# Performance work log

Hardware: AMD Instinct MI355X
Metric: run time of the kernel (lower is better)

## Reference

```python
import jax, jax.numpy as jnp
import numpy as np

EPS = 1e-6

def rmsnorm(x, w):
    # matches torch RMSNorm: normalize in fp32, cast back, scale
    xf = x.astype(jnp.float32)
    n = xf * jax.lax.rsqrt(jnp.mean(xf * xf, axis=-1, keepdims=True) + EPS)
    return n.astype(x.dtype) * w

def swiglu(x, w1, w2, w3):
    # torch Linear convention: weight shape [out, in], y = x @ W.T
    return (jax.nn.silu(x @ w1.T) * (x @ w3.T)) @ w2.T

B, D, E, K = 32768, 1024, 8, 2
NF = 4  # int(8 * 0.5) fractal experts, rest are plain SwiGLU(dim, 4*dim)

def setup_inputs() -> dict:
    key = jax.random.key(0)
    ks = jax.random.split(key, 8)
    def w(k, shape, fan_in):
        return jax.random.normal(k, shape, jnp.float32) * (fan_in ** -0.5)
    return {
        "x": jax.random.normal(ks[0], (B, D), jnp.float32),
        "gate_w": w(ks[1], (E, D), D),
        # FractalBlock experts (depth=1): RMSNorm weight, SwiGLU(dim, 2*dim), LayerScale gamma
        "fr_norm": jnp.ones((NF, D), jnp.float32),
        "fr_gamma": jnp.full((NF, D), 1e-5, jnp.float32),
        "fr_w1": w(ks[2], (NF, 2 * D, D), D),
        "fr_w2": w(ks[3], (NF, D, 2 * D), 2 * D),
        "fr_w3": w(ks[4], (NF, 2 * D, D), D),
        # Plain SwiGLU experts: SwiGLU(dim, 4*dim)
        "sw_w1": w(ks[5], (E - NF, 4 * D, D), D),
        "sw_w2": w(ks[6], (E - NF, D, 4 * D), 4 * D),
        "sw_w3": w(ks[7], (E - NF, 4 * D, D), D),
    }

def reference(x, gate_w, fr_norm, fr_gamma, fr_w1, fr_w2, fr_w3, sw_w1, sw_w2, sw_w3):
    n_experts = gate_w.shape[0]
    n_fractal = fr_w1.shape[0]
    # gating: softmax -> top-k -> renormalize selected weights
    probs = jax.nn.softmax(x @ gate_w.T, axis=-1)            # [B, E]
    tk_w, tk_i = jax.lax.top_k(probs, K)                     # [B, K]
    tk_w = tk_w / jnp.sum(tk_w, axis=-1, keepdims=True)
    # combine weights: zero for unselected experts (math identical to sparse dispatch)
    comb = jnp.sum(jax.nn.one_hot(tk_i, n_experts, dtype=x.dtype) * tk_w[..., None], axis=1)  # [B, E]
    out = jnp.zeros_like(x)
    for e in range(n_experts):  # fixed small structural loop over experts
        if e < n_fractal:
            # FractalBlock(depth=1), eval mode: stochastic depth is identity
            xn = rmsnorm(x, fr_norm[e])
            xn = xn + swiglu(xn, fr_w1[e], fr_w2[e], fr_w3[e])
            eo = fr_gamma[e] * xn + x
        else:
            j = e - n_fractal
            eo = swiglu(x, sw_w1[j], sw_w2[j], sw_w3[j])
        out = out + comb[:, e:e + 1] * eo
    return out
```

## Files before the change

### kernel.cpp

```cpp
#include <hip/hip_runtime.h>
#include <stdint.h>

#define B_TOK 32768
#define DIM   1024
#define NEXP  8
#define NFR   4
#define HF    2048
#define HS    4096
#define CT    64
#define NCH   9
#define PADROWS 66560

typedef __bf16 bf16;
typedef bf16  bf16x8 __attribute__((ext_vector_type(8)));
typedef bf16  bf16x4 __attribute__((ext_vector_type(4)));
typedef float f32x4  __attribute__((ext_vector_type(4)));

#define LDSOFF(R, CC) (((R) << 6) + ((((CC) ^ ((R) & 7))) << 3))

__global__ __launch_bounds__(256) void gate_kernel(
    const float* __restrict__ x, const float* __restrict__ gw_g,
    bf16* __restrict__ xb, float* __restrict__ rms,
    int* __restrict__ top2, float* __restrict__ c12) {
  __shared__ float gw[NEXP * DIM];
  for (int i = threadIdx.x; i < NEXP * DIM / 4; i += 256)
    *(f32x4*)(gw + i * 4) = *(const f32x4*)(gw_g + i * 4);
  __syncthreads();
  const int lane = threadIdx.x & 63;
  const int wave = threadIdx.x >> 6;
  const int row  = blockIdx.x * 4 + wave;
  const float* xr = x + (size_t)row * DIM;
  f32x4 xv[4];
#pragma unroll
  for (int i = 0; i < 4; i++) xv[i] = *(const f32x4*)(xr + lane * 4 + i * 256);
  float ss = 0.f;
  double dot[8] = {0, 0, 0, 0, 0, 0, 0, 0};
#pragma unroll
  for (int i = 0; i < 4; i++) {
#pragma unroll
    for (int c = 0; c < 4; c++) ss += xv[i][c] * xv[i][c];
#pragma unroll
    for (int e = 0; e < 8; e++) {
      const f32x4 g = *(const f32x4*)(gw + e * DIM + i * 256 + lane * 4);
#pragma unroll
      for (int c = 0; c < 4; c++) dot[e] += (double)xv[i][c] * (double)g[c];
    }
  }
#pragma unroll
  for (int off = 32; off > 0; off >>= 1) {
    ss += __shfl_xor(ss, off, 64);
#pragma unroll
    for (int e = 0; e < 8; e++) dot[e] += __shfl_xor(dot[e], off, 64);
  }
  const float rv = 1.0f / sqrtf(ss * (1.0f / DIM) + 1e-6f);
  if (lane == 0) rms[row] = rv;
  int i1 = 0; double m1 = dot[0];
#pragma unroll
  for (int e = 1; e < 8; e++) if (dot[e] > m1) { m1 = dot[e]; i1 = e; }
  int i2 = 0; double m2 = -1e300;
#pragma unroll
  for (int e = 0; e < 8; e++) if (e != i1 && dot[e] > m2) { m2 = dot[e]; i2 = e; }
  const double t  = exp(m2 - m1);
  if (lane == 0) {
    top2[row] = i1 | (i2 << 8);
    c12[2 * row]     = (float)(1.0 / (1.0 + t));
    c12[2 * row + 1] = (float)(t / (1.0 + t));
  }
#pragma unroll
  for (int i = 0; i < 4; i++) {
    bf16x4 o;
#pragma unroll
    for (int c = 0; c < 4; c++) o[c] = (bf16)xv[i][c];
    *(bf16x4*)(xb + (size_t)row * DIM + lane * 4 + i * 256) = o;
  }
}

__global__ __launch_bounds__(1024) void histoff_kernel(
    const int* __restrict__ top2, int* __restrict__ tileOff,
    int* __restrict__ rowOff) {
  __shared__ int h[8];
  if (threadIdx.x < 8) h[threadIdx.x] = 0;
  __syncthreads();
  int c[8] = {0, 0, 0, 0, 0, 0, 0, 0};
  for (int i = 0; i < B_TOK / 1024; i++) {
    const int pk = top2[threadIdx.x + i * 1024];
    const int e1 = pk & 255, e2 = pk >> 8;
#pragma unroll
    for (int e = 0; e < 8; e++) c[e] += (e1 == e) + (e2 == e);
  }
#pragma unroll
  for (int e = 0; e < 8; e++) {
#pragma unroll
    for (int off = 32; off > 0; off >>= 1) c[e] += __shfl_xor(c[e], off, 64);
  }
  if ((threadIdx.x & 63) == 0) {
#pragma unroll
    for (int e = 0; e < 8; e++) atomicAdd(&h[e], c[e]);
  }
  __syncthreads();
  if (threadIdx.x == 0) {
    int t = 0;
    for (int e = 0; e < 8; e++) {
      tileOff[e] = t;
      rowOff[e]  = t * 128;
      t += (h[e] + 127) >> 7;
    }
    tileOff[8] = t;
  }
}

__global__ __launch_bounds__(256) void assign_kernel(
    const int* __restrict__ top2, const float* __restrict__ c12,
    const int* __restrict__ rowOff, int* __restrict__ cur,
    int* __restrict__ perm, float* __restrict__ cwg) {
  __shared__ int lhist[8];
  __shared__ int lbase[8];
  if (threadIdx.x < 8) lhist[threadIdx.x] = 0;
  __syncthreads();
  const int t = blockIdx.x * 256 + threadIdx.x;
  const int pk = top2[t];
  const int e1 = pk & 255, e2 = pk >> 8;
  const int p1 = atomicAdd(&lhist[e1], 1);
  const int p2 = atomicAdd(&lhist[e2], 1);
  __syncthreads();
  if (threadIdx.x < 8) {
    const int c = lhist[threadIdx.x];
    lbase[threadIdx.x] = c ? atomicAdd(&cur[threadIdx.x * 32], c) : 0;
  }
  __syncthreads();
  const int g1 = rowOff[e1] + lbase[e1] + p1;
  perm[g1] = t; cwg[g1] = c12[2 * t];
  const int g2 = rowOff[e2] + lbase[e2] + p2;
  perm[g2] = t; cwg[g2] = c12[2 * t + 1];
}

__global__ __launch_bounds__(256) void cvt_kernel(
    const float* __restrict__ src, bf16* __restrict__ dst, int n4) {
  const int i = blockIdx.x * 256 + threadIdx.x;
  if (i >= n4) return;
  f32x4 v = *(const f32x4*)(src + (size_t)i * 4);
  *(bf16x4*)(dst + (size_t)i * 4) = __builtin_convertvector(v, bf16x4);
}

__global__ __launch_bounds__(256) void cvt_scaled_kernel(
    const float* __restrict__ src, const float* __restrict__ norm,
    bf16* __restrict__ dst, int n4) {
  const int i = blockIdx.x * 256 + threadIdx.x;
  if (i >= n4) return;
  const size_t f = (size_t)i * 4;
  f32x4 v = *(const f32x4*)(src + f);
  const float* np_ = norm + ((f >> 21) << 10) + (f & 1023);
#pragma unroll
  for (int c = 0; c < 4; c++) v[c] *= np_[c];
  *(bf16x4*)(dst + f) = __builtin_convertvector(v, bf16x4);
}

__device__ __forceinline__ void stage_sw(const bf16* __restrict__ g0, int ld,
                                         bf16* s0, int wave, int lane) {
  const int r = lane >> 3;
  const int c = (lane & 7) ^ r;
  const bf16* g = g0 + (size_t)(wave * 32 + r) * ld + c * 8;
  bf16* s = s0 + wave * 2048;
#pragma unroll
  for (int i = 0; i < 4; i++) {
    __builtin_amdgcn_global_load_lds(
        (const __attribute__((address_space(1))) void*)(uintptr_t)(g + (size_t)(i * 8) * ld),
        (__attribute__((address_space(3))) void*)(uintptr_t)(s + i * 512), 16, 0, 0);
  }
}

__global__ __launch_bounds__(256, 2) void gemm1_kernel(
    const bf16* __restrict__ xb, const int* __restrict__ perm,
    const float* __restrict__ rms,
    const bf16* __restrict__ fw1, const bf16* __restrict__ fw3,
    const bf16* __restrict__ s1b, const bf16* __restrict__ s3b,
    const int* __restrict__ tileOff, bf16* __restrict__ G, int chunk) {
  const int bt = chunk * CT + blockIdx.y;
  int toff[9];
#pragma unroll
  for (int i = 0; i < 9; i++) toff[i] = tileOff[i];
  if (bt >= toff[8]) return;
  int e = 0;
#pragma unroll
  for (int i = 1; i < 8; i++) if (bt >= toff[i]) e = i;
  const bool isfr = (e < NFR);
  const int nt = isfr ? 16 : 32;
  if ((int)blockIdx.x >= nt) return;
  const bf16* B1 = isfr ? fw1 + (size_t)e * HF * DIM : s1b + (size_t)(e - NFR) * HS * DIM;
  const bf16* B3 = isfr ? fw3 + (size_t)e * HF * DIM : s3b + (size_t)(e - NFR) * HS * DIM;

  __shared__ __attribute__((aligned(16))) bf16 As[128 * 64];
  __shared__ __attribute__((aligned(16))) bf16 Bs1[128 * 64];
  __shared__ __attribute__((aligned(16))) bf16 Bs3[128 * 64];
  const int lane = threadIdx.x & 63, wave = threadIdx.x >> 6;
  const int wm = wave >> 1, wn = wave & 1;
  const int g0 = bt * 128;
  const int n0 = blockIdx.x * 128;

  const int rA = lane >> 3;
  const int cA = (lane & 7) ^ rA;
  const bf16* Ag[4];
#pragma unroll
  for (int i = 0; i < 4; i++) {
    int tk = perm[g0 + wave * 32 + i * 8 + rA];
    if (tk < 0) tk = 0;
    Ag[i] = xb + (size_t)tk * DIM + cA * 8;
  }
  const bf16* B1b = B1 + (size_t)n0 * DIM;
  const bf16* B3b = B3 + (size_t)n0 * DIM;

  f32x4 acc1[4][4], acc3[4][4];
#pragma unroll
  for (int i = 0; i < 4; i++)
#pragma unroll
    for (int j = 0; j < 4; j++) {
      f32x4 z = {0.f, 0.f, 0.f, 0.f};
      acc1[i][j] = z; acc3[i][j] = z;
    }
  const int lr = lane & 15, lq = lane >> 4;
  bf16* Asw = As + wave * 2048;
  for (int k0 = 0; k0 < DIM; k0 += 64) {
#pragma unroll
    for (int i = 0; i < 4; i++) {
      __builtin_amdgcn_global_load_lds(
          (const __attribute__((address_space(1))) void*)(uintptr_t)(Ag[i] + k0),
          (__attribute__((address_space(3))) void*)(uintptr_t)(Asw + i * 512), 16, 0, 0);
    }
    stage_sw(B1b + k0, DIM, Bs1, wave, lane);
    stage_sw(B3b + k0, DIM, Bs3, wave, lane);
    __syncthreads();
#pragma unroll
    for (int ks = 0; ks < 2; ks++) {
      bf16x8 af[4], bf_[4], cf_[4];
#pragma unroll
      for (int mi = 0; mi < 4; mi++) {
        const int R = wm * 64 + mi * 16 + lr;
        af[mi] = *(const bf16x8*)(As + LDSOFF(R, ks * 4 + lq));
      }
#pragma unroll
      for (int ni = 0; ni < 4; ni++) {
        const int R = wn * 64 + ni * 16 + lr;
        bf_[ni] = *(const bf16x8*)(Bs1 + LDSOFF(R, ks * 4 + lq));
        cf_[ni] = *(const bf16x8*)(Bs3 + LDSOFF(R, ks * 4 + lq));
      }
#pragma unroll
      for (int mi = 0; mi < 4; mi++)
#pragma unroll
        for (int ni = 0; ni < 4; ni++) {
          acc1[mi][ni] = __builtin_amdgcn_mfma_f32_16x16x32_bf16(af[mi], bf_[ni], acc1[mi][ni], 0, 0, 0);
          acc3[mi][ni] = __builtin_amdgcn_mfma_f32_16x16x32_bf16(af[mi], cf_[ni], acc3[mi][ni], 0, 0, 0);
        }
    }
    __syncthreads();
  }
#pragma unroll
  for (int mi = 0; mi < 4; mi++) {
#pragma unroll
    for (int r = 0; r < 4; r++) {
      const int row_l = wm * 64 + mi * 16 + lq * 4 + r;
      float s = 1.0f;
      if (isfr) {
        int tok = perm[g0 + row_l];
        s = rms[tok < 0 ? 0 : tok];
      }
      bf16* Grow = G + (size_t)(blockIdx.y * 128 + row_l) * HS;
#pragma unroll
      for (int ni = 0; ni < 4; ni++) {
        const int col = n0 + wn * 64 + ni * 16 + lr;
        const float h1 = acc1[mi][ni][r] * s;
        const float h3 = acc3[mi][ni][r] * s;
        Grow[col] = (bf16)(h1 / (1.0f + __expf(-h1)) * h3);
      }
    }
  }
}

__global__ __launch_bounds__(256, 2) void gemm2_kernel(
    const bf16* __restrict__ G, const int* __restrict__ perm,
    const float* __restrict__ cwg, const float* __restrict__ rms,
    const float* __restrict__ gamma_all, const float* __restrict__ norm_all,
    const float* __restrict__ x,
    const bf16* __restrict__ fw2, const bf16* __restrict__ s2b,
    const int* __restrict__ tileOff, float* __restrict__ out, int chunk) {
  const int bt = chunk * CT + blockIdx.y;
  int toff[9];
#pragma unroll
  for (int i = 0; i < 9; i++) toff[i] = tileOff[i];
  if (bt >= toff[8]) return;
  int e = 0;
#pragma unroll
  for (int i = 1; i < 8; i++) if (bt >= toff[i]) e = i;
  const bool isfr = (e < NFR);
  const int K = isfr ? HF : HS;
  const bf16* Bw = isfr ? fw2 + (size_t)e * DIM * HF : s2b + (size_t)(e - NFR) * DIM * HS;

  __shared__ __attribute__((aligned(16))) bf16 As[128 * 64];
  __shared__ __attribute__((aligned(16))) bf16 Bs[128 * 64];
  const int lane = threadIdx.x & 63, wave = threadIdx.x >> 6;
  const int wm = wave >> 1, wn = wave & 1;
  const int n0 = blockIdx.x * 128;
  f32x4 acc[4][4];
#pragma unroll
  for (int i = 0; i < 4; i++)
#pragma unroll
    for (int j = 0; j < 4; j++) { f32x4 z = {0.f, 0.f, 0.f, 0.f}; acc[i][j] = z; }
  const bf16* Ab = G + (size_t)(blockIdx.y * 128) * HS;
  const bf16* Bb = Bw + (size_t)n0 * K;
  const int lr = lane & 15, lq = lane >> 4;
  for (int k0 = 0; k0 < K; k0 += 64) {
    stage_sw(Ab + k0, HS, As, wave, lane);
    stage_sw(Bb + k0, K, Bs, wave, lane);
    __syncthreads();
#pragma unroll
    for (int ks = 0; ks < 2; ks++) {
      bf16x8 af[4], bf_[4];
#pragma unroll
      for (int mi = 0; mi < 4; mi++) {
        const int R = wm * 64 + mi * 16 + lr;
        af[mi] = *(const bf16x8*)(As + LDSOFF(R, ks * 4 + lq));
      }
#pragma unroll
      for (int ni = 0; ni < 4; ni++) {
        const int R = wn * 64 + ni * 16 + lr;
        bf_[ni] = *(const bf16x8*)(Bs + LDSOFF(R, ks * 4 + lq));
      }
#pragma unroll
      for (int mi = 0; mi < 4; mi++)
#pragma unroll
        for (int ni = 0; ni < 4; ni++)
          acc[mi][ni] = __builtin_amdgcn_mfma_f32_16x16x32_bf16(af[mi], bf_[ni], acc[mi][ni], 0, 0, 0);
    }
    __syncthreads();
  }
#pragma unroll
  for (int mi = 0; mi < 4; mi++) {
#pragma unroll
    for (int r = 0; r < 4; r++) {
      const int row_l = wm * 64 + mi * 16 + lq * 4 + r;
      const int g_row = bt * 128 + row_l;
      const int tok = perm[g_row];
      if (tok < 0) continue;
      const float cw = cwg[g_row];
      const float rv = rms[tok];
#pragma unroll
      for (int ni = 0; ni < 4; ni++) {
        const int col = n0 + wn * 64 + ni * 16 + lr;
        const float a = acc[mi][ni][r];
        float res;
        if (isfr) {
          const float xvv = x[(size_t)tok * DIM + col];
          res = cw * (gamma_all[e * DIM + col] * (rv * xvv * norm_all[e * DIM + col] + a) + xvv);
        } else {
          res = cw * a;
        }
        atomicAdd(&out[(size_t)tok * DIM + col], res);
      }
    }
  }
}

extern "C" void kernel_launch(void* const* d_in, const int* in_sizes, int n_in,
                              void* d_out, int out_size, void* d_ws, size_t ws_size,
                              hipStream_t stream) {
  const float* x        = (const float*)d_in[0];
  const float* gate_w   = (const float*)d_in[1];
  const float* fr_norm  = (const float*)d_in[2];
  const float* fr_gamma = (const float*)d_in[3];
  const float* fr_w1    = (const float*)d_in[4];
  const float* fr_w2    = (const float*)d_in[5];
  const float* fr_w3    = (const float*)d_in[6];
  const float* sw_w1    = (const float*)d_in[7];
  const float* sw_w2    = (const float*)d_in[8];
  const float* sw_w3    = (const float*)d_in[9];
  float* out = (float*)d_out;

  char* ws = (char*)d_ws;
  bf16*  xb    = (bf16*)(ws);
  bf16*  fw1   = (bf16*)(ws + 67108864);
  bf16*  fw3   = (bf16*)(ws + 83886080);
  bf16*  fw2   = (bf16*)(ws + 100663296);
  bf16*  s1b   = (bf16*)(ws + 117440512);
  bf16*  s3b   = (bf16*)(ws + 150994944);
  bf16*  s2b   = (bf16*)(ws + 184549376);
  bf16*  G     = (bf16*)(ws + 218103808);
  float* rmsb  = (float*)(ws + 285212672);
  int*   top2  = (int*)  (ws + 285343744);
  float* c12   = (float*)(ws + 285474816);
  int*   perm  = (int*)  (ws + 285736960);
  float* cwg   = (float*)(ws + 286003200);
  int*   cur   = (int*)  (ws + 286269440);
  int*   tileOff = (int*)(ws + 286270464);
  int*   rowOff  = (int*)(ws + 286270500);

  hipMemsetAsync(d_out, 0, (size_t)out_size * sizeof(float), stream);
  hipMemsetAsync(cur, 0, 1024, stream);
  hipMemsetAsync(perm, 0xFF, PADROWS * 4, stream);

  gate_kernel<<<B_TOK / 4, 256, 0, stream>>>(x, gate_w, xb, rmsb, top2, c12);
  histoff_kernel<<<1, 1024, 0, stream>>>(top2, tileOff, rowOff);
  assign_kernel<<<B_TOK / 256, 256, 0, stream>>>(top2, c12, rowOff, cur, perm, cwg);

  cvt_scaled_kernel<<<8192, 256, 0, stream>>>(fr_w1, fr_norm, fw1, 2097152);
  cvt_scaled_kernel<<<8192, 256, 0, stream>>>(fr_w3, fr_norm, fw3, 2097152);
  cvt_kernel<<<8192, 256, 0, stream>>>(fr_w2, fw2, 2097152);
  cvt_kernel<<<16384, 256, 0, stream>>>(sw_w1, s1b, 4194304);
  cvt_kernel<<<16384, 256, 0, stream>>>(sw_w3, s3b, 4194304);
  cvt_kernel<<<16384, 256, 0, stream>>>(sw_w2, s2b, 4194304);

  for (int c = 0; c < NCH; c++) {
    gemm1_kernel<<<dim3(32, CT), 256, 0, stream>>>(
        xb, perm, rmsb, fw1, fw3, s1b, s3b, tileOff, G, c);
    gemm2_kernel<<<dim3(8, CT), 256, 0, stream>>>(
        G, perm, cwg, rmsb, fr_gamma, fr_norm, x, fw2, s2b, tileOff, out, c);
  }
}
```

Before: 2.741 ms.

## Interleave W1/W3 weights and use 256x256 double-buffered gemm1 tiles

Weight conversion now interleaves W1 and W3 rows in 16-row blocks into a single matrix, so gemm1 runs one fused GEMM where adjacent column fragments pair up for the SwiGLU epilogue. Gemm1 moves to 512-thread blocks with 256x256 tiles, double-buffered LDS staging and MFMA priority hints, to get more reuse per load and overlap global loads with compute. Expert row padding goes to 256, and gemm2 keeps 128-row tiles through a second offset table. The cost is more LDS and registers per block (32 accumulators per thread), which may lower occupancy, plus extra padding rows.

Result: no change. 2.728 ms (-0.5%).

```diff
diff --git a/kernel.cpp b/kernel.cpp
--- a/kernel.cpp
+++ b/kernel.cpp
@@ -7,9 +7,10 @@
 #define NFR   4
 #define HF    2048
 #define HS    4096
-#define CT    64
+#define CT1   32
+#define CT2   64
 #define NCH   9
-#define PADROWS 66560
+#define PADROWS 67584
 
 typedef __bf16 bf16;
 typedef bf16  bf16x8 __attribute__((ext_vector_type(8)));
@@ -76,8 +77,8 @@
 }
 
 __global__ __launch_bounds__(1024) void histoff_kernel(
-    const int* __restrict__ top2, int* __restrict__ tileOff,
-    int* __restrict__ rowOff) {
+    const int* __restrict__ top2, int* __restrict__ tileOff256,
+    int* __restrict__ tileOff128, int* __restrict__ rowOff) {
   __shared__ int h[8];
   if (threadIdx.x < 8) h[threadIdx.x] = 0;
   __syncthreads();
@@ -101,11 +102,13 @@
   if (threadIdx.x == 0) {
     int t = 0;
     for (int e = 0; e < 8; e++) {
-      tileOff[e] = t;
-      rowOff[e]  = t * 128;
-      t += (h[e] + 127) >> 7;
-    }
-    tileOff[8] = t;
+      tileOff256[e] = t;
+      tileOff128[e] = 2 * t;
+      rowOff[e]     = t * 256;
+      t += (h[e] + 255) >> 8;
+    }
+    tileOff256[8] = t;
+    tileOff128[8] = 2 * t;
   }
 }
 
@@ -142,17 +145,37 @@
   *(bf16x4*)(dst + (size_t)i * 4) = __builtin_convertvector(v, bf16x4);
 }
 
-__global__ __launch_bounds__(256) void cvt_scaled_kernel(
-    const float* __restrict__ src, const float* __restrict__ norm,
-    bf16* __restrict__ dst, int n4) {
+__global__ __launch_bounds__(256) void cvt_inter_fr(
+    const float* __restrict__ w1, const float* __restrict__ w3,
+    const float* __restrict__ norm, bf16* __restrict__ dst) {
   const int i = blockIdx.x * 256 + threadIdx.x;
-  if (i >= n4) return;
-  const size_t f = (size_t)i * 4;
-  f32x4 v = *(const f32x4*)(src + f);
-  const float* np_ = norm + ((f >> 21) << 10) + (f & 1023);
-#pragma unroll
-  for (int c = 0; c < 4; c++) v[c] *= np_[c];
-  *(bf16x4*)(dst + f) = __builtin_convertvector(v, bf16x4);
+  const int col4 = i & 255;
+  const int rp   = (i >> 8) & 4095;
+  const int e    = i >> 20;
+  const int blk  = rp >> 4;
+  const int sr   = ((blk >> 1) << 4) + (rp & 15);
+  const float* src = (blk & 1) ? w3 : w1;
+  f32x4 v  = *(const f32x4*)(src + ((size_t)e * HF + sr) * DIM + col4 * 4);
+  f32x4 nv = *(const f32x4*)(norm + e * DIM + col4 * 4);
+#pragma unroll
+  for (int c = 0; c < 4; c++) v[c] *= nv[c];
+  *(bf16x4*)(dst + ((size_t)e * 4096 + rp) * DIM + col4 * 4) =
+      __builtin_convertvector(v, bf16x4);
+}
+
+__global__ __launch_bounds__(256) void cvt_inter_sw(
+    const float* __restrict__ w1, const float* __restrict__ w3,
+    bf16* __restrict__ dst) {
+  const int i = blockIdx.x * 256 + threadIdx.x;
+  const int col4 = i & 255;
+  const int rp   = (i >> 8) & 8191;
+  const int e    = i >> 21;
+  const int blk  = rp >> 4;
+  const int sr   = ((blk >> 1) << 4) + (rp & 15);
+  const float* src = (blk & 1) ? w3 : w1;
+  f32x4 v = *(const f32x4*)(src + ((size_t)e * HS + sr) * DIM + col4 * 4);
+  *(bf16x4*)(dst + ((size_t)e * 8192 + rp) * DIM + col4 * 4) =
+      __builtin_convertvector(v, bf16x4);
 }
 
 __device__ __forceinline__ void stage_sw(const bf16* __restrict__ g0, int ld,
@@ -169,16 +192,15 @@
   }
 }
 
-__global__ __launch_bounds__(256, 2) void gemm1_kernel(
+__global__ __launch_bounds__(512, 2) void gemm1_kernel(
     const bf16* __restrict__ xb, const int* __restrict__ perm,
     const float* __restrict__ rms,
-    const bf16* __restrict__ fw1, const bf16* __restrict__ fw3,
-    const bf16* __restrict__ s1b, const bf16* __restrict__ s3b,
-    const int* __restrict__ tileOff, bf16* __restrict__ G, int chunk) {
-  const int bt = chunk * CT + blockIdx.y;
+    const bf16* __restrict__ fwi, const bf16* __restrict__ swi,
+    const int* __restrict__ tileOff256, bf16* __restrict__ G, int chunk) {
+  const int bt = chunk * CT1 + blockIdx.y;
   int toff[9];
 #pragma unroll
-  for (int i = 0; i < 9; i++) toff[i] = tileOff[i];
+  for (int i = 0; i < 9; i++) toff[i] = tileOff256[i];
   if (bt >= toff[8]) return;
   int e = 0;
 #pragma unroll
@@ -186,16 +208,15 @@
   const bool isfr = (e < NFR);
   const int nt = isfr ? 16 : 32;
   if ((int)blockIdx.x >= nt) return;
-  const bf16* B1 = isfr ? fw1 + (size_t)e * HF * DIM : s1b + (size_t)(e - NFR) * HS * DIM;
-  const bf16* B3 = isfr ? fw3 + (size_t)e * HF * DIM : s3b + (size_t)(e - NFR) * HS * DIM;
-
-  __shared__ __attribute__((aligned(16))) bf16 As[128 * 64];
-  __shared__ __attribute__((aligned(16))) bf16 Bs1[128 * 64];
-  __shared__ __attribute__((aligned(16))) bf16 Bs3[128 * 64];
+  const bf16* Bp = isfr ? fwi + (size_t)e * 4096 * DIM
+                        : swi + (size_t)(e - NFR) * 8192 * DIM;
+
+  __shared__ __attribute__((aligned(16))) bf16 As[2 * 16384];
+  __shared__ __attribute__((aligned(16))) bf16 Bs[2 * 16384];
   const int lane = threadIdx.x & 63, wave = threadIdx.x >> 6;
-  const int wm = wave >> 1, wn = wave & 1;
-  const int g0 = bt * 128;
-  const int n0 = blockIdx.x * 128;
+  const int wm = wave >> 2, wn = wave & 3;
+  const int g0  = bt * 256;
+  const int n0p = blockIdx.x * 256;
 
   const int rA = lane >> 3;
   const int cA = (lane & 7) ^ rA;
@@ -206,69 +227,81 @@
     if (tk < 0) tk = 0;
     Ag[i] = xb + (size_t)tk * DIM + cA * 8;
   }
-  const bf16* B1b = B1 + (size_t)n0 * DIM;
-  const bf16* B3b = B3 + (size_t)n0 * DIM;
-
-  f32x4 acc1[4][4], acc3[4][4];
-#pragma unroll
-  for (int i = 0; i < 4; i++)
-#pragma unroll
-    for (int j = 0; j < 4; j++) {
-      f32x4 z = {0.f, 0.f, 0.f, 0.f};
-      acc1[i][j] = z; acc3[i][j] = z;
-    }
+  const bf16* Bg = Bp + (size_t)(n0p + wave * 32 + rA) * DIM + cA * 8;
+
+  f32x4 acc[8][4];
+#pragma unroll
+  for (int i = 0; i < 8; i++)
+#pragma unroll
+    for (int j = 0; j < 4; j++) { f32x4 z = {0.f, 0.f, 0.f, 0.f}; acc[i][j] = z; }
   const int lr = lane & 15, lq = lane >> 4;
-  bf16* Asw = As + wave * 2048;
-  for (int k0 = 0; k0 < DIM; k0 += 64) {
+
+  auto stage = [&](int buf, int k0) {
+    bf16* sa = As + buf * 16384 + wave * 2048;
+    bf16* sb = Bs + buf * 16384 + wave * 2048;
 #pragma unroll
     for (int i = 0; i < 4; i++) {
       __builtin_amdgcn_global_load_lds(
           (const __attribute__((address_space(1))) void*)(uintptr_t)(Ag[i] + k0),
-          (__attribute__((address_space(3))) void*)(uintptr_t)(Asw + i * 512), 16, 0, 0);
-    }
-    stage_sw(B1b + k0, DIM, Bs1, wave, lane);
-    stage_sw(B3b + k0, DIM, Bs3, wave, lane);
-    __syncthreads();
+          (__attribute__((address_space(3))) void*)(uintptr_t)(sa + i * 512), 16, 0, 0);
+    }
+#pragma unroll
+    for (int i = 0; i < 4; i++) {
+      __builtin_amdgcn_global_load_lds(
+          (const __attribute__((address_space(1))) void*)(uintptr_t)(Bg + (size_t)(i * 8) * DIM + k0),
+          (__attribute__((address_space(3))) void*)(uintptr_t)(sb + i * 512), 16, 0, 0);
+    }
+  };
+  auto compute = [&](int buf) {
+    const bf16* Ab = As + buf * 16384;
+    const bf16* Bb = Bs + buf * 16384;
 #pragma unroll
     for (int ks = 0; ks < 2; ks++) {
-      bf16x8 af[4], bf_[4], cf_[4];
-#pragma unroll
-      for (int mi = 0; mi < 4; mi++) {
-        const int R = wm * 64 + mi * 16 + lr;
-        af[mi] = *(const bf16x8*)(As + LDSOFF(R, ks * 4 + lq));
-      }
-#pragma unroll
-      for (int ni = 0; ni < 4; ni++) {
-        const int R = wn * 64 + ni * 16 + lr;
-        bf_[ni] = *(const bf16x8*)(Bs1 + LDSOFF(R, ks * 4 + lq));
-        cf_[ni] = *(const bf16x8*)(Bs3 + LDSOFF(R, ks * 4 + lq));
-      }
-#pragma unroll
-      for (int mi = 0; mi < 4; mi++)
-#pragma unroll
-        for (int ni = 0; ni < 4; ni++) {
-          acc1[mi][ni] = __builtin_amdgcn_mfma_f32_16x16x32_bf16(af[mi], bf_[ni], acc1[mi][ni], 0, 0, 0);
-          acc3[mi][ni] = __builtin_amdgcn_mfma_f32_16x16x32_bf16(af[mi], cf_[ni], acc3[mi][ni], 0, 0, 0);
-        }
-    }
-    __syncthreads();
-  }
-#pragma unroll
-  for (int mi = 0; mi < 4; mi++) {
+      bf16x8 af[8], bfv[4];
+#pragma unroll
+      for (int mi = 0; mi < 8; mi++)
+        af[mi] = *(const bf16x8*)(Ab + LDSOFF(wm * 128 + mi * 16 + lr, ks * 4 + lq));
+#pragma unroll
+      for (int ni = 0; ni < 4; ni++)
+        bfv[ni] = *(const bf16x8*)(Bb + LDSOFF(wn * 64 + ni * 16 + lr, ks * 4 + lq));
+      __builtin_amdgcn_s_setprio(1);
+#pragma unroll
+      for (int mi = 0; mi < 8; mi++)
+#pragma unroll
+        for (int ni = 0; ni < 4; ni++)
+          acc[mi][ni] = __builtin_amdgcn_mfma_f32_16x16x32_bf16(af[mi], bfv[ni], acc[mi][ni], 0, 0, 0);
+      __builtin_amdgcn_s_setprio(0);
+    }
+  };
+
+  stage(0, 0);
+  __syncthreads();
+  int k = 64;
+#pragma unroll 1
+  for (int t = 0; t < 7; t++) {
+    stage(1, k); compute(0); __syncthreads(); k += 64;
+    stage(0, k); compute(1); __syncthreads(); k += 64;
+  }
+  stage(1, k); compute(0); __syncthreads();
+  compute(1);
+
+  const int gh = n0p >> 1;
+#pragma unroll
+  for (int mi = 0; mi < 8; mi++) {
 #pragma unroll
     for (int r = 0; r < 4; r++) {
-      const int row_l = wm * 64 + mi * 16 + lq * 4 + r;
+      const int row_l = wm * 128 + mi * 16 + lq * 4 + r;
       float s = 1.0f;
       if (isfr) {
         int tok = perm[g0 + row_l];
         s = rms[tok < 0 ? 0 : tok];
       }
-      bf16* Grow = G + (size_t)(blockIdx.y * 128 + row_l) * HS;
-#pragma unroll
-      for (int ni = 0; ni < 4; ni++) {
-        const int col = n0 + wn * 64 + ni * 16 + lr;
-        const float h1 = acc1[mi][ni][r] * s;
-        const float h3 = acc3[mi][ni][r] * s;
+      bf16* Grow = G + (size_t)(blockIdx.y * 256 + row_l) * HS;
+#pragma unroll
+      for (int nh = 0; nh < 2; nh++) {
+        const float h1 = acc[mi][2 * nh][r] * s;
+        const float h3 = acc[mi][2 * nh + 1][r] * s;
+        const int col = gh + wn * 32 + nh * 16 + lr;
         Grow[col] = (bf16)(h1 / (1.0f + __expf(-h1)) * h3);
       }
     }
@@ -281,11 +314,11 @@
     const float* __restrict__ gamma_all, const float* __restrict__ norm_all,
     const float* __restrict__ x,
     const bf16* __restrict__ fw2, const bf16* __restrict__ s2b,
-    const int* __restrict__ tileOff, float* __restrict__ out, int chunk) {
-  const int bt = chunk * CT + blockIdx.y;
+    const int* __restrict__ tileOff128, float* __restrict__ out, int chunk) {
+  const int bt = chunk * CT2 + blockIdx.y;
   int toff[9];
 #pragma unroll
-  for (int i = 0; i < 9; i++) toff[i] = tileOff[i];
+  for (int i = 0; i < 9; i++) toff[i] = tileOff128[i];
   if (bt >= toff[8]) return;
   int e = 0;
 #pragma unroll
@@ -376,41 +409,38 @@
 
   char* ws = (char*)d_ws;
   bf16*  xb    = (bf16*)(ws);
-  bf16*  fw1   = (bf16*)(ws + 67108864);
-  bf16*  fw3   = (bf16*)(ws + 83886080);
+  bf16*  fwi   = (bf16*)(ws + 67108864);
   bf16*  fw2   = (bf16*)(ws + 100663296);
-  bf16*  s1b   = (bf16*)(ws + 117440512);
-  bf16*  s3b   = (bf16*)(ws + 150994944);
+  bf16*  swi   = (bf16*)(ws + 117440512);
   bf16*  s2b   = (bf16*)(ws + 184549376);
   bf16*  G     = (bf16*)(ws + 218103808);
   float* rmsb  = (float*)(ws + 285212672);
   int*   top2  = (int*)  (ws + 285343744);
   float* c12   = (float*)(ws + 285474816);
   int*   perm  = (int*)  (ws + 285736960);
-  float* cwg   = (float*)(ws + 286003200);
-  int*   cur   = (int*)  (ws + 286269440);
-  int*   tileOff = (int*)(ws + 286270464);
-  int*   rowOff  = (int*)(ws + 286270500);
+  float* cwg   = (float*)(ws + 286007296);
+  int*   cur   = (int*)  (ws + 286277632);
+  int*   tileOff256 = (int*)(ws + 286278656);
+  int*   tileOff128 = (int*)(ws + 286278720);
+  int*   rowOff     = (int*)(ws + 286278784);
 
   hipMemsetAsync(d_out, 0, (size_t)out_size * sizeof(float), stream);
   hipMemsetAsync(cur, 0, 1024, stream);
   hipMemsetAsync(perm, 0xFF, PADROWS * 4, stream);
 
   gate_kernel<<<B_TOK / 4, 256, 0, stream>>>(x, gate_w, xb, rmsb, top2, c12);
-  histoff_kernel<<<1, 1024, 0, stream>>>(top2, tileOff, rowOff);
+  histoff_kernel<<<1, 1024, 0, stream>>>(top2, tileOff256, tileOff128, rowOff);
   assign_kernel<<<B_TOK / 256, 256, 0, stream>>>(top2, c12, rowOff, cur, perm, cwg);
 
-  cvt_scaled_kernel<<<8192, 256, 0, stream>>>(fr_w1, fr_norm, fw1, 2097152);
-  cvt_scaled_kernel<<<8192, 256, 0, stream>>>(fr_w3, fr_norm, fw3, 2097152);
+  cvt_inter_fr<<<16384, 256, 0, stream>>>(fr_w1, fr_w3, fr_norm, fwi);
   cvt_kernel<<<8192, 256, 0, stream>>>(fr_w2, fw2, 2097152);
-  cvt_kernel<<<16384, 256, 0, stream>>>(sw_w1, s1b, 4194304);
-  cvt_kernel<<<16384, 256, 0, stream>>>(sw_w3, s3b, 4194304);
+  cvt_inter_sw<<<32768, 256, 0, stream>>>(sw_w1, sw_w3, swi);
   cvt_kernel<<<16384, 256, 0, stream>>>(sw_w2, s2b, 4194304);
 
   for (int c = 0; c < NCH; c++) {
-    gemm1_kernel<<<dim3(32, CT), 256, 0, stream>>>(
-        xb, perm, rmsb, fw1, fw3, s1b, s3b, tileOff, G, c);
-    gemm2_kernel<<<dim3(8, CT), 256, 0, stream>>>(
-        G, perm, cwg, rmsb, fr_gamma, fr_norm, x, fw2, s2b, tileOff, out, c);
-  }
-}
+    gemm1_kernel<<<dim3(32, CT1), 512, 0, stream>>>(
+        xb, perm, rmsb, fwi, swi, tileOff256, G, c);
+    gemm2_kernel<<<dim3(8, CT2), 256, 0, stream>>>(
+        G, perm, cwg, rmsb, fr_gamma, fr_norm, x, fw2, s2b, tileOff128, out, c);
+  }
+}
```
